# Performance work log

Measured on AMD Instinct MI355X. Metric: run time of the kernel, lower is better.

## Reference

```python
import jax, jax.numpy as jnp
import numpy as np

# BEV grid parameters from calculate_birds_eye_view_parameters([-50,50,0.5],[-50,50,0.5],[-10,10,20])
BEV_RES = np.array([0.5, 0.5, 20.0], dtype=np.float32)
BEV_START = np.array([-49.75, -49.75, 0.0], dtype=np.float32)   # lower + res/2
BEV_DIM = (200, 200, 1)                                          # (X, Y, Z)

B, N, D, H, W, C = 2, 6, 48, 28, 60, 64


def setup_inputs() -> dict:
    key = jax.random.key(0)
    k1, k2, k3 = jax.random.split(key, 3)
    x = jax.random.normal(k1, (B, N, D, H, W, C), dtype=jnp.float32)
    geo_xy = jax.random.uniform(k2, (B, N, D, H, W, 2), minval=-55.0, maxval=55.0)
    geo_z = jax.random.uniform(k3, (B, N, D, H, W, 1), minval=-12.0, maxval=12.0)
    geometry = jnp.concatenate([geo_xy, geo_z], axis=-1).astype(jnp.float32)
    return {"x": x, "geometry": geometry}


def reference(x, geometry):
    # x:        [B, N, D, H, W, C] camera frustum features
    # geometry: [B, N, D, H, W, 3] ego-frame (x, y, z) of each frustum point
    b, n, d, h, w, c = x.shape
    res = jnp.asarray(BEV_RES)
    start = jnp.asarray(BEV_START)
    dim = jnp.asarray(BEV_DIM, dtype=jnp.int32)
    X, Y, Z = BEV_DIM
    nvox = X * Y * Z

    # voxel index; torch .long() truncates toward zero -> astype(int32) matches
    vox = ((geometry - (start - res / 2.0)) / res).astype(jnp.int32)   # [B,N,D,H,W,3]
    vox = vox.reshape(b, -1, 3)                                        # [B, Np, 3]
    feat = x.reshape(b, -1, c)                                         # [B, Np, C]

    valid = jnp.all((vox >= 0) & (vox < dim), axis=-1)                 # [B, Np]
    ranks = vox[..., 0] * (Y * Z) + vox[..., 1] * Z + vox[..., 2]      # [B, Np]
    seg = jnp.where(valid, ranks + jnp.arange(b, dtype=jnp.int32)[:, None] * nvox,
                    b * nvox)                                          # invalid -> dump segment

    # per-voxel sum == sorted cumsum + dedup-diff of VoxelsSumming
    pooled = jax.ops.segment_sum(feat.reshape(-1, c), seg.reshape(-1),
                                 num_segments=b * nvox + 1)            # [B*nvox+1, C]
    bev = pooled[: b * nvox].reshape(b, X, Y, Z, c)                    # [B, X, Y, Z, C]
    # torch scatters into [Z, X, Y, C], permutes to [Z, C, X, Y], squeezes Z=1 -> [B, C, X, Y]
    out = bev.transpose(0, 3, 4, 1, 2).reshape(b, Z * c, X, Y)
    return out
```

## Files before the change

### kernel.cpp

```cpp
#include <hip/hip_runtime.h>

#define Bq 2
#define Nn 6
#define Dd 48
#define Hh 28
#define Ww 60
#define Cc 64
#define Xd 200
#define Yd 200
#define NP (Nn*Dd*Hh*Ww)
#define TOTP (Bq*NP)
#define NVOX (Xd*Yd)
#define NSEG (Bq*NVOX)
#define NB1  79
#define CAP  512
#define RND  32

__global__ __launch_bounds__(1024) void zero_cnt(int* __restrict__ cnt)
{
    int i = blockIdx.x * 1024 + threadIdx.x;
    if (i < NSEG) cnt[i] = 0;
}

__global__ __launch_bounds__(256) void phase_a(
    const float* __restrict__ geom, int* __restrict__ rank, int* __restrict__ cnt)
{
    int p = blockIdx.x * 256 + threadIdx.x;
    if (p >= TOTP) return;
    float gx = geom[(long)p*3 + 0];
    float gy = geom[(long)p*3 + 1];
    float gz = geom[(long)p*3 + 2];
    int vx = (int)((gx + 50.0f) / 0.5f);
    int vy = (int)((gy + 50.0f) / 0.5f);
    int vz = (int)((gz + 10.0f) / 20.0f);
    int seg = -1;
    if (vx >= 0 && vx < Xd && vy >= 0 && vy < Yd && vz == 0) {
        int b = (p >= NP) ? 1 : 0;
        seg = b * NVOX + vx * Yd + vy;
        atomicAdd(&cnt[seg], 1);
    }
    rank[p] = seg;
}

__global__ __launch_bounds__(1024) void scan_p1(
    const int* __restrict__ cnt, int* __restrict__ start, int* __restrict__ bsum)
{
    __shared__ int sh[1024];
    int tid = threadIdx.x;
    int i = blockIdx.x * 1024 + tid;
    int v = (i < NSEG) ? cnt[i] : 0;
    sh[tid] = v;
    __syncthreads();
    for (int off = 1; off < 1024; off <<= 1) {
        int t = (tid >= off) ? sh[tid - off] : 0;
        __syncthreads();
        sh[tid] += t;
        __syncthreads();
    }
    if (i < NSEG) start[i] = sh[tid] - v;
    if (tid == 1023) bsum[blockIdx.x] = sh[1023];
}

__global__ __launch_bounds__(128) void scan_p2(int* __restrict__ bsum)
{
    __shared__ int sh[128];
    int tid = threadIdx.x;
    int v = (tid < NB1) ? bsum[tid] : 0;
    sh[tid] = v;
    __syncthreads();
    for (int off = 1; off < 128; off <<= 1) {
        int t = (tid >= off) ? sh[tid - off] : 0;
        __syncthreads();
        sh[tid] += t;
        __syncthreads();
    }
    if (tid < NB1) bsum[tid] = sh[tid] - v;
}

__global__ __launch_bounds__(1024) void scan_p3(
    int* __restrict__ start, const int* __restrict__ bsum)
{
    int i = blockIdx.x * 1024 + threadIdx.x;
    if (i < NSEG) start[i] += bsum[blockIdx.x];
}

__global__ __launch_bounds__(256) void phase_c(
    const int* __restrict__ rank, int* __restrict__ start, int* __restrict__ order)
{
    int p = blockIdx.x * 256 + threadIdx.x;
    if (p >= TOTP) return;
    int seg = rank[p];
    if (seg < 0) return;
    int pos = atomicAdd(&start[seg], 1);
    order[pos] = p;
}

#define DMA_ROW(gp, lp) \
    __builtin_amdgcn_global_load_lds( \
        (const __attribute__((address_space(1))) void*)(gp), \
        (__attribute__((address_space(3))) void*)(lp), 4, 0, 0)

__global__ __launch_bounds__(256) void phase_d(
    const int* __restrict__ endp, const int* __restrict__ order,
    const float* __restrict__ x, float* __restrict__ out)
{
    __shared__ int   ord_sh[4][CAP];
    __shared__ float pbuf[4][RND][Cc];
    __shared__ float tile[32][68];
    int blk  = blockIdx.x;
    int b    = blk / (NVOX/32);
    int xy0  = (blk % (NVOX/32)) * 32;
    int wv   = threadIdx.x >> 6;
    int lane = threadIdx.x & 63;
    int seg0 = b * NVOX + xy0 + wv * 8;

    int e = 0;
    if (lane < 9) {
        int idx = seg0 - 1 + lane;
        e = (idx >= 0) ? endp[idx] : 0;
    }
    int eb0 = __shfl(e, 0);
    int rb[9];
    #pragma unroll
    for (int j = 0; j < 9; ++j) rb[j] = __shfl(e, j) - eb0;
    int count = rb[8];

    int g = lane >> 4;
    int q = (lane & 15) * 4;

    float4 A[8];
    #pragma unroll
    for (int v = 0; v < 8; ++v) A[v] = make_float4(0.f, 0.f, 0.f, 0.f);

    if (count <= CAP) {
        for (int i = lane; i < count; i += 64)
            ord_sh[wv][i] = order[eb0 + i];

        for (int base = 0; base < count; base += RND) {
            int n = count - base; if (n > RND) n = RND;
            int pidv = 0;
            if (lane < RND) pidv = ord_sh[wv][base + lane];
            #pragma unroll
            for (int j = 0; j < RND; ++j) {
                if (base + j < count) {
                    int spid = __builtin_amdgcn_readlane(pidv, j);
                    const float* gp = x + (size_t)spid * Cc + lane;
                    DMA_ROW(gp, &pbuf[wv][j][0]);
                }
            }
            asm volatile("s_waitcnt vmcnt(0)" ::: "memory");
            #pragma unroll
            for (int v = 0; v < 8; ++v) {
                int lo = rb[v]   - base; if (lo < 0) lo = 0;
                int hi = rb[v+1] - base; if (hi > n) hi = n;
                for (int t = lo + g; t < hi; t += 4) {
                    const float4 a = *(const float4*)&pbuf[wv][t][q];
                    A[v].x += a.x; A[v].y += a.y;
                    A[v].z += a.z; A[v].w += a.w;
                }
            }
        }
    } else {
        #pragma unroll
        for (int v = 0; v < 8; ++v) {
            int begin = eb0 + rb[v];
            int endv  = eb0 + rb[v+1];
            for (int t = begin + g; t < endv; t += 4) {
                int p0 = order[t];
                const float4 a0 = *(const float4*)(x + (long)p0 * Cc + q);
                A[v].x += a0.x; A[v].y += a0.y;
                A[v].z += a0.z; A[v].w += a0.w;
            }
        }
    }

    #pragma unroll
    for (int v = 0; v < 8; ++v) {
        A[v].x += __shfl_xor(A[v].x, 16); A[v].y += __shfl_xor(A[v].y, 16);
        A[v].z += __shfl_xor(A[v].z, 16); A[v].w += __shfl_xor(A[v].w, 16);
        A[v].x += __shfl_xor(A[v].x, 32); A[v].y += __shfl_xor(A[v].y, 32);
        A[v].z += __shfl_xor(A[v].z, 32); A[v].w += __shfl_xor(A[v].w, 32);
    }
    if (g == 0) {
        #pragma unroll
        for (int v = 0; v < 8; ++v)
            *(float4*)&tile[wv*8 + v][q] = A[v];
    }
    __syncthreads();

    float* dst = out + (long)b * Cc * NVOX + xy0;
    int xy = threadIdx.x & 31;
    int c0 = threadIdx.x >> 5;
    #pragma unroll
    for (int s = 0; s < 8; ++s) {
        int c = s * 8 + c0;
        dst[(long)c * NVOX + xy] = tile[xy][c];
    }
}

__global__ __launch_bounds__(256) void fiery_scatter_direct(
    const float* __restrict__ x, const float* __restrict__ geom,
    float* __restrict__ out)
{
    int wid  = blockIdx.x * 4 + (threadIdx.x >> 6);
    int lane = threadIdx.x & 63;
    if (wid >= TOTP) return;
    long gb = (long)wid * 3;
    float gx = geom[gb+0], gy = geom[gb+1], gz = geom[gb+2];
    int vx = (int)((gx + 50.0f) / 0.5f);
    int vy = (int)((gy + 50.0f) / 0.5f);
    int vz = (int)((gz + 10.0f) / 20.0f);
    if (!(vx >= 0 && vx < Xd && vy >= 0 && vy < Yd && vz == 0)) return;
    int b = (wid >= NP) ? 1 : 0;
    float vv = x[(long)wid * Cc + lane];
    long dst = ((long)(b * Cc + lane)) * NVOX + (vx * Yd + vy);
    atomicAdd(&out[dst], vv);
}

extern "C" void kernel_launch(void* const* d_in, const int* in_sizes, int n_in,
                              void* d_out, int out_size, void* d_ws, size_t ws_size,
                              hipStream_t stream)
{
    const float* x    = (const float*)d_in[0];
    const float* geom = (const float*)d_in[1];
    float* out = (float*)d_out;

    size_t need = ((size_t)TOTP * 2 + (size_t)NSEG * 2 + 128) * sizeof(int);
    if (ws_size >= need) {
        int* rank  = (int*)d_ws;
        int* order = rank  + TOTP;
        int* cnt   = order + TOTP;
        int* start = cnt   + NSEG;
        int* bsum  = start + NSEG;

        zero_cnt<<<NB1, 1024, 0, stream>>>(cnt);
        phase_a<<<TOTP/256, 256, 0, stream>>>(geom, rank, cnt);
        scan_p1<<<NB1, 1024, 0, stream>>>(cnt, start, bsum);
        scan_p2<<<1, 128, 0, stream>>>(bsum);
        scan_p3<<<NB1, 1024, 0, stream>>>(start, bsum);
        phase_c<<<TOTP/256, 256, 0, stream>>>(rank, start, order);
        phase_d<<<Bq*(NVOX/32), 256, 0, stream>>>(start, order, x, out);
    } else {
        hipMemsetAsync(out, 0, (size_t)out_size * sizeof(float), stream);
        fiery_scatter_direct<<<TOTP/4, 256, 0, stream>>>(x, geom, out);
    }
}
```

Before: 134.2 us.

## Replace LDS DMA staging with direct unrolled float4 gathers, halve block size

The gather phase no longer stages feature rows into LDS through global_load_lds with a full vmcnt wait. Each wave now reads point indices from shared memory and issues direct float4 global loads, unrolled by two per 4-lane group to keep more loads in flight. Blocks shrink to 128 threads covering 16 voxels, which lowers LDS use and should raise occupancy. The output transpose writes float4 nontemporal stores per channel. The inline capacity drops to 256 points per wave, so denser voxel runs fall back to the slower global-index path.

```diff
diff --git a/kernel.cpp b/kernel.cpp
--- a/kernel.cpp
+++ b/kernel.cpp
@@ -13,8 +13,9 @@
 #define NVOX (Xd*Yd)
 #define NSEG (Bq*NVOX)
 #define NB1  79
-#define CAP  512
-#define RND  32
+#define CAP  256
+
+typedef float f32x4 __attribute__((ext_vector_type(4)));
 
 __global__ __launch_bounds__(1024) void zero_cnt(int* __restrict__ cnt)
 {
@@ -95,21 +96,15 @@
     order[pos] = p;
 }
 
-#define DMA_ROW(gp, lp) \
-    __builtin_amdgcn_global_load_lds( \
-        (const __attribute__((address_space(1))) void*)(gp), \
-        (__attribute__((address_space(3))) void*)(lp), 4, 0, 0)
-
-__global__ __launch_bounds__(256) void phase_d(
+__global__ __launch_bounds__(128) void phase_d(
     const int* __restrict__ endp, const int* __restrict__ order,
     const float* __restrict__ x, float* __restrict__ out)
 {
-    __shared__ int   ord_sh[4][CAP];
-    __shared__ float pbuf[4][RND][Cc];
-    __shared__ float tile[32][68];
+    __shared__ int   ord_sh[2][CAP];
+    __shared__ float tile[16][68];
     int blk  = blockIdx.x;
-    int b    = blk / (NVOX/32);
-    int xy0  = (blk % (NVOX/32)) * 32;
+    int b    = blk / (NVOX/16);
+    int xy0  = (blk % (NVOX/16)) * 16;
     int wv   = threadIdx.x >> 6;
     int lane = threadIdx.x & 63;
     int seg0 = b * NVOX + xy0 + wv * 8;
@@ -135,41 +130,33 @@
     if (count <= CAP) {
         for (int i = lane; i < count; i += 64)
             ord_sh[wv][i] = order[eb0 + i];
-
-        for (int base = 0; base < count; base += RND) {
-            int n = count - base; if (n > RND) n = RND;
-            int pidv = 0;
-            if (lane < RND) pidv = ord_sh[wv][base + lane];
-            #pragma unroll
-            for (int j = 0; j < RND; ++j) {
-                if (base + j < count) {
-                    int spid = __builtin_amdgcn_readlane(pidv, j);
-                    const float* gp = x + (size_t)spid * Cc + lane;
-                    DMA_ROW(gp, &pbuf[wv][j][0]);
-                }
+        #pragma unroll
+        for (int v = 0; v < 8; ++v) {
+            int re = rb[v + 1];
+            int t  = rb[v] + g;
+            for (; t + 4 < re; t += 8) {
+                int p0 = ord_sh[wv][t];
+                int p1 = ord_sh[wv][t + 4];
+                const float4 a0 = *(const float4*)(x + (long)p0 * Cc + q);
+                const float4 a1 = *(const float4*)(x + (long)p1 * Cc + q);
+                A[v].x += a0.x + a1.x; A[v].y += a0.y + a1.y;
+                A[v].z += a0.z + a1.z; A[v].w += a0.w + a1.w;
             }
-            asm volatile("s_waitcnt vmcnt(0)" ::: "memory");
-            #pragma unroll
-            for (int v = 0; v < 8; ++v) {
-                int lo = rb[v]   - base; if (lo < 0) lo = 0;
-                int hi = rb[v+1] - base; if (hi > n) hi = n;
-                for (int t = lo + g; t < hi; t += 4) {
-                    const float4 a = *(const float4*)&pbuf[wv][t][q];
-                    A[v].x += a.x; A[v].y += a.y;
-                    A[v].z += a.z; A[v].w += a.w;
-                }
+            if (t < re) {
+                int p0 = ord_sh[wv][t];
+                const float4 a0 = *(const float4*)(x + (long)p0 * Cc + q);
+                A[v].x += a0.x; A[v].y += a0.y; A[v].z += a0.z; A[v].w += a0.w;
             }
         }
     } else {
         #pragma unroll
         for (int v = 0; v < 8; ++v) {
             int begin = eb0 + rb[v];
-            int endv  = eb0 + rb[v+1];
+            int endv  = eb0 + rb[v + 1];
             for (int t = begin + g; t < endv; t += 4) {
                 int p0 = order[t];
                 const float4 a0 = *(const float4*)(x + (long)p0 * Cc + q);
-                A[v].x += a0.x; A[v].y += a0.y;
-                A[v].z += a0.z; A[v].w += a0.w;
+                A[v].x += a0.x; A[v].y += a0.y; A[v].z += a0.z; A[v].w += a0.w;
             }
         }
     }
@@ -188,14 +175,15 @@
     }
     __syncthreads();
 
-    float* dst = out + (long)b * Cc * NVOX + xy0;
-    int xy = threadIdx.x & 31;
-    int c0 = threadIdx.x >> 5;
-    #pragma unroll
-    for (int s = 0; s < 8; ++s) {
-        int c = s * 8 + c0;
-        dst[(long)c * NVOX + xy] = tile[xy][c];
-    }
+    int c  = threadIdx.x & 63;
+    int hv = threadIdx.x >> 6;
+    float4 w0 = make_float4(tile[hv*8+0][c], tile[hv*8+1][c],
+                            tile[hv*8+2][c], tile[hv*8+3][c]);
+    float4 w1 = make_float4(tile[hv*8+4][c], tile[hv*8+5][c],
+                            tile[hv*8+6][c], tile[hv*8+7][c]);
+    float* dst = out + (long)b * Cc * NVOX + (long)c * NVOX + xy0 + hv*8;
+    __builtin_nontemporal_store(*(f32x4*)&w0, (f32x4*)dst);
+    __builtin_nontemporal_store(*(f32x4*)&w1, (f32x4*)(dst + 4));
 }
 
 __global__ __launch_bounds__(256) void fiery_scatter_direct(
@@ -239,7 +227,7 @@
         scan_p2<<<1, 128, 0, stream>>>(bsum);
         scan_p3<<<NB1, 1024, 0, stream>>>(start, bsum);
         phase_c<<<TOTP/256, 256, 0, stream>>>(rank, start, order);
-        phase_d<<<Bq*(NVOX/32), 256, 0, stream>>>(start, order, x, out);
+        phase_d<<<Bq*(NVOX/16), 128, 0, stream>>>(start, order, x, out);
     } else {
         hipMemsetAsync(out, 0, (size_t)out_size * sizeof(float), stream);
         fiery_scatter_direct<<<TOTP/4, 256, 0, stream>>>(x, geom, out);
```

Result: slower. 137.2 us (+2.2%).

## Convert valid point features to fp16 before the per-voxel gather-sum

Applied to the files above, without the earlier changes.

Adds a pass that reads the features of every valid point once and writes them as packed fp16 into workspace. The gather kernel then reads half-width rows through the sorted order instead of staging fp32 rows into LDS with async global-to-LDS copies, and accumulates in fp32. The aim is to halve the random-gather traffic in the reduction. The price is an extra full read of x plus a write of the fp16 copy, and a loss of precision from rounding inputs to fp16, which may miss the reference tolerance.

```diff
diff --git a/kernel.cpp b/kernel.cpp
--- a/kernel.cpp
+++ b/kernel.cpp
@@ -14,7 +14,8 @@
 #define NSEG (Bq*NVOX)
 #define NB1  79
 #define CAP  512
-#define RND  32
+
+typedef float f32x4 __attribute__((ext_vector_type(4)));
 
 __global__ __launch_bounds__(1024) void zero_cnt(int* __restrict__ cnt)
 {
@@ -95,17 +96,38 @@
     order[pos] = p;
 }
 
-#define DMA_ROW(gp, lp) \
-    __builtin_amdgcn_global_load_lds( \
-        (const __attribute__((address_space(1))) void*)(gp), \
-        (__attribute__((address_space(3))) void*)(lp), 4, 0, 0)
+__global__ __launch_bounds__(256) void conv_f16(
+    const int* __restrict__ rank, const float* __restrict__ x,
+    unsigned int* __restrict__ xh)
+{
+    int w    = blockIdx.x * 4 + (threadIdx.x >> 6);
+    int lane = threadIdx.x & 63;
+    int sub  = lane >> 4;
+    int li   = lane & 15;
+    int p    = 4 * w + sub;
+    if (rank[p] < 0) return;
+
+    const f32x4 v = __builtin_nontemporal_load(
+        (const f32x4*)(x + (size_t)p * Cc + 4 * li));
+    _Float16 h0 = (_Float16)v[0], h1 = (_Float16)v[1];
+    _Float16 h2 = (_Float16)v[2], h3 = (_Float16)v[3];
+    unsigned int u0 = (unsigned int)__builtin_bit_cast(unsigned short, h0)
+                    | ((unsigned int)__builtin_bit_cast(unsigned short, h1) << 16);
+    unsigned int u1 = (unsigned int)__builtin_bit_cast(unsigned short, h2)
+                    | ((unsigned int)__builtin_bit_cast(unsigned short, h3) << 16);
+    *(uint2*)(xh + (size_t)p * 32 + 2 * li) = make_uint2(u0, u1);
+}
+
+#define H2F(u) ((float)__builtin_bit_cast(_Float16, (unsigned short)(u)))
+#define ADDU2(AK, wq) { \
+    AK.x += H2F((wq).x & 0xffffu); AK.y += H2F((wq).x >> 16); \
+    AK.z += H2F((wq).y & 0xffffu); AK.w += H2F((wq).y >> 16); }
 
 __global__ __launch_bounds__(256) void phase_d(
     const int* __restrict__ endp, const int* __restrict__ order,
-    const float* __restrict__ x, float* __restrict__ out)
+    const unsigned int* __restrict__ xh, float* __restrict__ out)
 {
     __shared__ int   ord_sh[4][CAP];
-    __shared__ float pbuf[4][RND][Cc];
     __shared__ float tile[32][68];
     int blk  = blockIdx.x;
     int b    = blk / (NVOX/32);
@@ -125,51 +147,46 @@
     for (int j = 0; j < 9; ++j) rb[j] = __shfl(e, j) - eb0;
     int count = rb[8];
 
-    int g = lane >> 4;
-    int q = (lane & 15) * 4;
+    int g   = lane >> 4;
+    int l15 = lane & 15;
+    int q   = l15 * 4;
 
     float4 A[8];
     #pragma unroll
     for (int v = 0; v < 8; ++v) A[v] = make_float4(0.f, 0.f, 0.f, 0.f);
+
+    const uint2* xh2 = (const uint2*)xh;
 
     if (count <= CAP) {
         for (int i = lane; i < count; i += 64)
             ord_sh[wv][i] = order[eb0 + i];
-
-        for (int base = 0; base < count; base += RND) {
-            int n = count - base; if (n > RND) n = RND;
-            int pidv = 0;
-            if (lane < RND) pidv = ord_sh[wv][base + lane];
-            #pragma unroll
-            for (int j = 0; j < RND; ++j) {
-                if (base + j < count) {
-                    int spid = __builtin_amdgcn_readlane(pidv, j);
-                    const float* gp = x + (size_t)spid * Cc + lane;
-                    DMA_ROW(gp, &pbuf[wv][j][0]);
-                }
+        #pragma unroll
+        for (int v = 0; v < 8; ++v) {
+            int re = rb[v + 1];
+            int t  = rb[v] + g;
+            for (; t + 4 < re; t += 8) {
+                int p0 = ord_sh[wv][t];
+                int p1 = ord_sh[wv][t + 4];
+                const uint2 a0 = xh2[(size_t)p0 * 16 + l15];
+                const uint2 a1 = xh2[(size_t)p1 * 16 + l15];
+                ADDU2(A[v], a0);
+                ADDU2(A[v], a1);
             }
-            asm volatile("s_waitcnt vmcnt(0)" ::: "memory");
-            #pragma unroll
-            for (int v = 0; v < 8; ++v) {
-                int lo = rb[v]   - base; if (lo < 0) lo = 0;
-                int hi = rb[v+1] - base; if (hi > n) hi = n;
-                for (int t = lo + g; t < hi; t += 4) {
-                    const float4 a = *(const float4*)&pbuf[wv][t][q];
-                    A[v].x += a.x; A[v].y += a.y;
-                    A[v].z += a.z; A[v].w += a.w;
-                }
+            if (t < re) {
+                int p0 = ord_sh[wv][t];
+                const uint2 a0 = xh2[(size_t)p0 * 16 + l15];
+                ADDU2(A[v], a0);
             }
         }
     } else {
         #pragma unroll
         for (int v = 0; v < 8; ++v) {
             int begin = eb0 + rb[v];
-            int endv  = eb0 + rb[v+1];
+            int endv  = eb0 + rb[v + 1];
             for (int t = begin + g; t < endv; t += 4) {
                 int p0 = order[t];
-                const float4 a0 = *(const float4*)(x + (long)p0 * Cc + q);
-                A[v].x += a0.x; A[v].y += a0.y;
-                A[v].z += a0.z; A[v].w += a0.w;
+                const uint2 a0 = xh2[(size_t)p0 * 16 + l15];
+                ADDU2(A[v], a0);
             }
         }
     }
@@ -225,13 +242,15 @@
     const float* geom = (const float*)d_in[1];
     float* out = (float*)d_out;
 
-    size_t need = ((size_t)TOTP * 2 + (size_t)NSEG * 2 + 128) * sizeof(int);
+    size_t need = ((size_t)TOTP * 2 + (size_t)NSEG * 2 + 128) * sizeof(int)
+                + (size_t)TOTP * 32 * sizeof(unsigned int);
     if (ws_size >= need) {
         int* rank  = (int*)d_ws;
         int* order = rank  + TOTP;
         int* cnt   = order + TOTP;
         int* start = cnt   + NSEG;
         int* bsum  = start + NSEG;
+        unsigned int* xh = (unsigned int*)(bsum + 128);
 
         zero_cnt<<<NB1, 1024, 0, stream>>>(cnt);
         phase_a<<<TOTP/256, 256, 0, stream>>>(geom, rank, cnt);
@@ -239,7 +258,8 @@
         scan_p2<<<1, 128, 0, stream>>>(bsum);
         scan_p3<<<NB1, 1024, 0, stream>>>(start, bsum);
         phase_c<<<TOTP/256, 256, 0, stream>>>(rank, start, order);
-        phase_d<<<Bq*(NVOX/32), 256, 0, stream>>>(start, order, x, out);
+        conv_f16<<<TOTP/16, 256, 0, stream>>>(rank, x, xh);
+        phase_d<<<Bq*(NVOX/32), 256, 0, stream>>>(start, order, xh, out);
     } else {
         hipMemsetAsync(out, 0, (size_t)out_size * sizeof(float), stream);
         fiery_scatter_direct<<<TOTP/4, 256, 0, stream>>>(x, geom, out);
```

Measured after the change: 174.3 us. 1.3x slower.
